# Performance work log

Hardware: AMD Instinct MI355X
Metric: run time of the kernel (lower is better)

The kernel has to match this reference:

```python
import jax, jax.numpy as jnp
import numpy as np
import math

H = 16
D_MODEL = 1024
D_K = D_MODEL // H
B, S = 4, 2048
NEG = -1.0e9


def setup_inputs() -> dict:
    key = jax.random.key(0)
    ks = jax.random.split(key, 13)
    scale = 1.0 / math.sqrt(D_MODEL)
    inp = {
        "query": jax.random.normal(ks[0], (B, S, D_MODEL), jnp.float32),
        "key": jax.random.normal(ks[1], (B, S, D_MODEL), jnp.float32),
        "value": jax.random.normal(ks[2], (B, S, D_MODEL), jnp.float32),
        "mask": jax.random.randint(ks[3], (B, S), 0, 2, jnp.int32),
        "Wq": jax.random.normal(ks[4], (D_MODEL, D_MODEL), jnp.float32) * scale,
        "bq": jax.random.normal(ks[5], (D_MODEL,), jnp.float32) * scale,
        "Wk": jax.random.normal(ks[6], (D_MODEL, D_MODEL), jnp.float32) * scale,
        "bk": jax.random.normal(ks[7], (D_MODEL,), jnp.float32) * scale,
        "Wv": jax.random.normal(ks[8], (D_MODEL, D_MODEL), jnp.float32) * scale,
        "bv": jax.random.normal(ks[9], (D_MODEL,), jnp.float32) * scale,
        "Wo": jax.random.normal(ks[10], (D_MODEL, D_MODEL), jnp.float32) * scale,
        "bo": jax.random.normal(ks[11], (D_MODEL,), jnp.float32) * scale,
    }
    return inp


def _split_heads(x):
    # [B, S, D] -> [B, H, S, D_K]
    b, s, _ = x.shape
    return x.reshape(b, s, H, D_K).transpose(0, 2, 1, 3)


def reference(query, key, value, mask, Wq, bq, Wk, bk, Wv, bv, Wo, bo):
    # torch nn.Linear: y = x @ W.T + b
    q = _split_heads(query @ Wq.T + bq)
    k = _split_heads(key @ Wk.T + bk)
    v = _split_heads(value @ Wv.T + bv)
    scores = jnp.einsum("bhqd,bhkd->bhqk", q, k) / math.sqrt(D_K)
    # [B, S] key-padding mask -> broadcast as [B, 1, 1, S] (== torch's [B,1,S,S] repeat)
    m = mask[:, None, None, :]
    scores = jnp.where(m == 0, NEG, scores)
    p = jax.nn.softmax(scores, axis=-1)
    out = jnp.einsum("bhqk,bhkd->bhqd", p, v)  # [B, H, S, D_K]
    out = out.transpose(0, 2, 1, 3).reshape(query.shape[0], -1, D_MODEL)
    return out @ Wo.T + bo
```

## Files before the change

### kernel.cpp

```cpp
#include <hip/hip_runtime.h>


#define DMODEL 1024
#define SLEN 2048
#define NHEAD 16
#define LOG2E 1.44269504088896340736f

typedef __attribute__((ext_vector_type(4))) float f32x4;
typedef __attribute__((ext_vector_type(8))) short bf16x8;
typedef __attribute__((ext_vector_type(4))) int i32x4;
typedef __attribute__((ext_vector_type(2))) int i32x2;

__device__ __forceinline__ unsigned short f2bf(float f) {
  __bf16 h = (__bf16)f;
  union { __bf16 h; unsigned short u; } cv; cv.h = h; return cv.u;
}
__device__ __forceinline__ unsigned pk(float a, float b) {
  return (unsigned)f2bf(a) | ((unsigned)f2bf(b) << 16);
}
__device__ __forceinline__ float fexp2(float x) {
#if __has_builtin(__builtin_amdgcn_exp2f)
  return __builtin_amdgcn_exp2f(x);
#else
  return exp2f(x);
#endif
}
__device__ __forceinline__ f32x4 zero4() {
  f32x4 z; z[0] = 0.f; z[1] = 0.f; z[2] = 0.f; z[3] = 0.f; return z;
}
__device__ __forceinline__ void gload16(const void* g, void* l) {
  __builtin_amdgcn_global_load_lds(
      (const __attribute__((address_space(1))) unsigned int*)(uintptr_t)g,
      (__attribute__((address_space(3))) unsigned int*)(uintptr_t)l, 16, 0, 0);
}

__global__ __launch_bounds__(256)
void gemm_qkv(const float* __restrict__ xq, const float* __restrict__ xk,
              const float* __restrict__ xv,
              const float* __restrict__ Wq, const float* __restrict__ bq,
              const float* __restrict__ Wk, const float* __restrict__ bk,
              const float* __restrict__ Wv, const float* __restrict__ bv,
              unsigned short* __restrict__ qw, unsigned short* __restrict__ kw,
              unsigned short* __restrict__ vw)
{
  const int z = blockIdx.z;
  const float* __restrict__ X    = (z == 0) ? xq : (z == 1) ? xk : xv;
  const float* __restrict__ W    = (z == 0) ? Wq : (z == 1) ? Wk : Wv;
  const float* __restrict__ bias = (z == 0) ? bq : (z == 1) ? bk : bv;
  const float scale = (z == 0) ? 0.125f * LOG2E : 1.0f;

  const int n0 = blockIdx.x * 128;
  const int m0 = blockIdx.y * 128;
  const int tid = threadIdx.x;
  const int lane = tid & 63, wid = tid >> 6;
  const int l15 = lane & 15, g = lane >> 4;
  const int wr = wid >> 1, wc = wid & 1;

  __shared__ __align__(16) unsigned short SM[2 * 128 * 40];
  unsigned short* Al = SM;
  unsigned short* Bl = SM + 128 * 40;
  unsigned short* TT = SM;

  const int srow = tid >> 1, sh = tid & 1;
  const float* __restrict__ Ag = X + (size_t)(m0 + srow) * DMODEL + sh * 16;
  const float* __restrict__ Bg = W + (size_t)(n0 + srow) * DMODEL + sh * 16;

  f32x4 acc[4][4];
#pragma unroll
  for (int i = 0; i < 4; ++i)
#pragma unroll
    for (int j = 0; j < 4; ++j) acc[i][j] = zero4();

  f32x4 ar[4], br[4];
#pragma unroll
  for (int i = 0; i < 4; ++i) {
    ar[i] = *(const f32x4*)(Ag + i * 4);
    br[i] = *(const f32x4*)(Bg + i * 4);
  }

  for (int kk = 0; kk < 32; ++kk) {
    __syncthreads();
    i32x4 wa0, wa1, wb0, wb1;
    wa0[0] = pk(ar[0][0], ar[0][1]); wa0[1] = pk(ar[0][2], ar[0][3]);
    wa0[2] = pk(ar[1][0], ar[1][1]); wa0[3] = pk(ar[1][2], ar[1][3]);
    wa1[0] = pk(ar[2][0], ar[2][1]); wa1[1] = pk(ar[2][2], ar[2][3]);
    wa1[2] = pk(ar[3][0], ar[3][1]); wa1[3] = pk(ar[3][2], ar[3][3]);
    wb0[0] = pk(br[0][0], br[0][1]); wb0[1] = pk(br[0][2], br[0][3]);
    wb0[2] = pk(br[1][0], br[1][1]); wb0[3] = pk(br[1][2], br[1][3]);
    wb1[0] = pk(br[2][0], br[2][1]); wb1[1] = pk(br[2][2], br[2][3]);
    wb1[2] = pk(br[3][0], br[3][1]); wb1[3] = pk(br[3][2], br[3][3]);
    *(i32x4*)&Al[srow * 40 + sh * 16]     = wa0;
    *(i32x4*)&Al[srow * 40 + sh * 16 + 8] = wa1;
    *(i32x4*)&Bl[srow * 40 + sh * 16]     = wb0;
    *(i32x4*)&Bl[srow * 40 + sh * 16 + 8] = wb1;
    __syncthreads();
    if (kk < 31) {
      const float* Ap = Ag + (kk + 1) * 32;
      const float* Bp = Bg + (kk + 1) * 32;
#pragma unroll
      for (int i = 0; i < 4; ++i) {
        ar[i] = *(const f32x4*)(Ap + i * 4);
        br[i] = *(const f32x4*)(Bp + i * 4);
      }
    }
    bf16x8 afr[4], bfr[4];
#pragma unroll
    for (int i = 0; i < 4; ++i) {
      afr[i] = *(const bf16x8*)&Al[(wr * 64 + i * 16 + l15) * 40 + g * 8];
      bfr[i] = *(const bf16x8*)&Bl[(wc * 64 + i * 16 + l15) * 40 + g * 8];
    }
#pragma unroll
    for (int mi = 0; mi < 4; ++mi)
#pragma unroll
      for (int ni = 0; ni < 4; ++ni)
        acc[mi][ni] = __builtin_amdgcn_mfma_f32_16x16x32_bf16(
            afr[mi], bfr[ni], acc[mi][ni], 0, 0, 0);
  }

  float bv4[4];
#pragma unroll
  for (int ni = 0; ni < 4; ++ni) bv4[ni] = bias[n0 + wc * 64 + ni * 16 + l15];

  if (z == 2) {
    const int bb = m0 >> 11, s0 = m0 & 2047;
#pragma unroll
    for (int p = 0; p < 2; ++p) {
      __syncthreads();
      if (wc == p) {
#pragma unroll
        for (int mi = 0; mi < 4; ++mi)
#pragma unroll
          for (int ni = 0; ni < 4; ++ni)
#pragma unroll
            for (int r = 0; r < 4; ++r)
              TT[(ni * 16 + l15) * 136 + wr * 64 + mi * 16 + 4 * g + r] =
                  f2bf(acc[mi][ni][r] + bv4[ni]);
      }
      __syncthreads();
      const int rr = tid >> 2, cc = (tid & 3) * 32;
      unsigned short* dp = vw + ((size_t)(bb * 1024 + n0 + p * 64 + rr)) * 2048 + s0 + cc;
      const unsigned short* sp = &TT[rr * 136 + cc];
#pragma unroll
      for (int j = 0; j < 4; ++j)
        *(i32x4*)(void*)(dp + j * 8) = *(const i32x4*)(const void*)(sp + j * 8);
    }
    return;
  }

  unsigned short* __restrict__ dst = (z == 0) ? qw : kw;
#pragma unroll
  for (int mi = 0; mi < 4; ++mi) {
#pragma unroll
    for (int ni = 0; ni < 4; ++ni) {
      const int n = n0 + wc * 64 + ni * 16 + l15;
      const int h = n >> 6, d = n & 63;
#pragma unroll
      for (int r = 0; r < 4; ++r) {
        const int m = m0 + wr * 64 + mi * 16 + 4 * g + r;
        const int b = m >> 11, s = m & 2047;
        const float val = (acc[mi][ni][r] + bv4[ni]) * scale;
        dst[((size_t)(b * NHEAD + h) * SLEN + s) * 64 + d] = f2bf(val);
      }
    }
  }
}

__global__ __launch_bounds__(256, 3)
void attn(const unsigned short* __restrict__ q_ws,
          const unsigned short* __restrict__ k_ws,
          const unsigned short* __restrict__ vT,
          const int* __restrict__ mask,
          unsigned short* __restrict__ o_ws)
{
  const int bh = blockIdx.x;
  const int qt = blockIdx.y;
  const int b = bh >> 4, h = bh & 15;
  const int tid = threadIdx.x, w = tid >> 6, lane = tid & 63;
  const int l15 = lane & 15, g = lane >> 4;

  __shared__ __align__(16) unsigned short Kb[2][64 * 64];
  __shared__ __align__(16) unsigned short Vb[2][64 * 64];
  __shared__ __align__(16) unsigned short Pl[4][16 * 64];
  __shared__ __align__(16) float maskf[2048];

  {
    const int4* mp = (const int4*)(mask + b * SLEN);
    const int4 ma = mp[tid * 2], mb = mp[tid * 2 + 1];
    float4 f0, f1;
    f0.x = ma.x ? 0.f : -1e9f; f0.y = ma.y ? 0.f : -1e9f;
    f0.z = ma.z ? 0.f : -1e9f; f0.w = ma.w ? 0.f : -1e9f;
    f1.x = mb.x ? 0.f : -1e9f; f1.y = mb.y ? 0.f : -1e9f;
    f1.z = mb.z ? 0.f : -1e9f; f1.w = mb.w ? 0.f : -1e9f;
    *(float4*)&maskf[tid * 8]     = f0;
    *(float4*)&maskf[tid * 8 + 4] = f1;
  }

  const size_t head = (size_t)bh * SLEN;
  const int r8 = lane >> 3, c8 = lane & 7;
  const int swz = ((c8 ^ r8) * 16);
  const unsigned pswz = (unsigned)((l15 & 7) << 4);

  const int qbase = qt * 128 + w * 32;
  bf16x8 qf[2][2];
  {
    const unsigned short* qp0 = q_ws + (head + qbase + l15) * 64;
    const unsigned short* qp1 = q_ws + (head + qbase + 16 + l15) * 64;
    qf[0][0] = *(const bf16x8*)(qp0 + g * 8);
    qf[0][1] = *(const bf16x8*)(qp0 + 32 + g * 8);
    qf[1][0] = *(const bf16x8*)(qp1 + g * 8);
    qf[1][1] = *(const bf16x8*)(qp1 + 32 + g * 8);
  }

  auto stage = [&](int kt2, int bufi) {
#pragma unroll
    for (int cl = 0; cl < 2; ++cl) {
      const int r = w * 16 + cl * 8 + r8;
      const char* gk = (const char*)(k_ws + (head + kt2 * 64 + r) * 64) + swz;
      gload16(gk, &Kb[bufi][(w * 16 + cl * 8) * 64]);
      const char* gv = (const char*)(vT + ((size_t)(bh * 64 + r)) * SLEN + kt2 * 64) + swz;
      gload16(gv, &Vb[bufi][(w * 16 + cl * 8) * 64]);
    }
  };

  stage(0, 0);
  __syncthreads();

  float m_run[2] = {-1e30f, -1e30f};
  float l_run[2] = {0.f, 0.f};
  f32x4 of[2][4];
#pragma unroll
  for (int qi = 0; qi < 2; ++qi)
#pragma unroll
    for (int n = 0; n < 4; ++n) of[qi][n] = zero4();

  unsigned short* Pw = (unsigned short*)Pl[w];
  int cur = 0;

  for (int kt = 0; kt < 32; ++kt) {
    if (kt + 1 < 32) stage(kt + 1, cur ^ 1);
    const char* Kc = (const char*)Kb[cur];
    const char* Vc = (const char*)Vb[cur];
    const int kv0 = kt * 64;

    f32x4 mv[4];
#pragma unroll
    for (int s = 0; s < 4; ++s) mv[s] = *(const f32x4*)&maskf[kv0 + s * 16 + g * 4];

#pragma unroll
    for (int qi = 0; qi < 2; ++qi) {
      f32x4 sac[4];
#pragma unroll
      for (int s = 0; s < 4; ++s) {
        const char* kr = Kc + (s * 16 + l15) * 128;
        const bf16x8 kf0 = *(const bf16x8*)(kr + ((unsigned)(g * 16) ^ pswz));
        const bf16x8 kf1 = *(const bf16x8*)(kr + ((unsigned)(64 + g * 16) ^ pswz));
        f32x4 zt = mv[s];
        zt = __builtin_amdgcn_mfma_f32_16x16x32_bf16(kf0, qf[qi][0], zt, 0, 0, 0);
        sac[s] = __builtin_amdgcn_mfma_f32_16x16x32_bf16(kf1, qf[qi][1], zt, 0, 0, 0);
      }

      float tmax = -3.0e38f;
#pragma unroll
      for (int s = 0; s < 4; ++s)
#pragma unroll
        for (int r = 0; r < 4; ++r) tmax = fmaxf(tmax, sac[s][r]);
      tmax = fmaxf(tmax, __shfl_xor(tmax, 16));
      tmax = fmaxf(tmax, __shfl_xor(tmax, 32));
      if (!__all(tmax <= m_run[qi] + 8.f)) {
        const float mnew = fmaxf(m_run[qi], tmax);
        const float alpha = fexp2(m_run[qi] - mnew);
        float af[4];
#pragma unroll
        for (int r = 0; r < 4; ++r) af[r] = __shfl(alpha, g * 4 + r);
#pragma unroll
        for (int n = 0; n < 4; ++n)
#pragma unroll
          for (int r = 0; r < 4; ++r) of[qi][n][r] *= af[r];
        l_run[qi] *= alpha;
        m_run[qi] = mnew;
      }
      float psum = 0.f;
      unsigned pr[4][2];
#pragma unroll
      for (int s = 0; s < 4; ++s) {
        const float p0 = fexp2(sac[s][0] - m_run[qi]);
        const float p1 = fexp2(sac[s][1] - m_run[qi]);
        const float p2 = fexp2(sac[s][2] - m_run[qi]);
        const float p3 = fexp2(sac[s][3] - m_run[qi]);
        psum += (p0 + p1) + (p2 + p3);
        pr[s][0] = pk(p0, p1); pr[s][1] = pk(p2, p3);
      }
      l_run[qi] += psum;
#pragma unroll
      for (int s = 0; s < 4; ++s) {
        i32x2 wv; wv[0] = (int)pr[s][0]; wv[1] = (int)pr[s][1];
        *(i32x2*)(void*)((char*)Pw + l15 * 128 + ((unsigned)(s * 32 + g * 8) ^ pswz)) = wv;
      }

#pragma unroll
      for (int k2 = 0; k2 < 2; ++k2) {
        const bf16x8 pa = *(const bf16x8*)(const void*)(
            (const char*)Pw + l15 * 128 + ((unsigned)(k2 * 64 + g * 16) ^ pswz));
#pragma unroll
        for (int n = 0; n < 4; ++n) {
          const bf16x8 vf = *(const bf16x8*)(
              Vc + (n * 16 + l15) * 128 + ((unsigned)(k2 * 64 + g * 16) ^ pswz));
          of[qi][n] = __builtin_amdgcn_mfma_f32_16x16x32_bf16(pa, vf, of[qi][n], 0, 0, 0);
        }
      }
    }
    __syncthreads();
    cur ^= 1;
  }

#pragma unroll
  for (int qi = 0; qi < 2; ++qi) {
    float lt = l_run[qi];
    lt += __shfl_xor(lt, 16);
    lt += __shfl_xor(lt, 32);
    float inv[4];
#pragma unroll
    for (int r = 0; r < 4; ++r) inv[r] = 1.f / __shfl(lt, g * 4 + r);
    const int qrow0 = qt * 128 + w * 32 + qi * 16;
#pragma unroll
    for (int n = 0; n < 4; ++n) {
      const int d = h * 64 + n * 16 + l15;
#pragma unroll
      for (int r = 0; r < 4; ++r) {
        const int sr = qrow0 + 4 * g + r;
        o_ws[((size_t)b * SLEN + sr) * DMODEL + d] = f2bf(of[qi][n][r] * inv[r]);
      }
    }
  }
}

__global__ __launch_bounds__(256)
void gemm_out(const unsigned short* __restrict__ ow,
              const float* __restrict__ Wo, const float* __restrict__ bo,
              float* __restrict__ out)
{
  const int n0 = blockIdx.x * 128;
  const int m0 = blockIdx.y * 128;
  const int tid = threadIdx.x;
  const int lane = tid & 63, wid = tid >> 6;
  const int l15 = lane & 15, g = lane >> 4;
  const int wr = wid >> 1, wc = wid & 1;

  __shared__ __align__(16) unsigned short Al[128 * 40];
  __shared__ __align__(16) unsigned short Bl[128 * 40];

  const int srow = tid >> 1, sh = tid & 1;
  const unsigned short* __restrict__ Ag = ow + (size_t)(m0 + srow) * DMODEL + sh * 16;
  const float* __restrict__ Bg = Wo + (size_t)(n0 + srow) * DMODEL + sh * 16;

  f32x4 acc[4][4];
#pragma unroll
  for (int i = 0; i < 4; ++i)
#pragma unroll
    for (int j = 0; j < 4; ++j) acc[i][j] = zero4();

  i32x4 ar0 = *(const i32x4*)Ag;
  i32x4 ar1 = *(const i32x4*)(Ag + 8);
  f32x4 br[4];
#pragma unroll
  for (int i = 0; i < 4; ++i) br[i] = *(const f32x4*)(Bg + i * 4);

  for (int kk = 0; kk < 32; ++kk) {
    __syncthreads();
    i32x4 wb0, wb1;
    wb0[0] = pk(br[0][0], br[0][1]); wb0[1] = pk(br[0][2], br[0][3]);
    wb0[2] = pk(br[1][0], br[1][1]); wb0[3] = pk(br[1][2], br[1][3]);
    wb1[0] = pk(br[2][0], br[2][1]); wb1[1] = pk(br[2][2], br[2][3]);
    wb1[2] = pk(br[3][0], br[3][1]); wb1[3] = pk(br[3][2], br[3][3]);
    *(i32x4*)&Al[srow * 40 + sh * 16]     = ar0;
    *(i32x4*)&Al[srow * 40 + sh * 16 + 8] = ar1;
    *(i32x4*)&Bl[srow * 40 + sh * 16]     = wb0;
    *(i32x4*)&Bl[srow * 40 + sh * 16 + 8] = wb1;
    __syncthreads();
    if (kk < 31) {
      const unsigned short* Ap = Ag + (kk + 1) * 32;
      const float* Bp = Bg + (kk + 1) * 32;
      ar0 = *(const i32x4*)Ap;
      ar1 = *(const i32x4*)(Ap + 8);
#pragma unroll
      for (int i = 0; i < 4; ++i) br[i] = *(const f32x4*)(Bp + i * 4);
    }
    bf16x8 afr[4], bfr[4];
#pragma unroll
    for (int i = 0; i < 4; ++i) {
      afr[i] = *(const bf16x8*)&Al[(wr * 64 + i * 16 + l15) * 40 + g * 8];
      bfr[i] = *(const bf16x8*)&Bl[(wc * 64 + i * 16 + l15) * 40 + g * 8];
    }
#pragma unroll
    for (int mi = 0; mi < 4; ++mi)
#pragma unroll
      for (int ni = 0; ni < 4; ++ni)
        acc[mi][ni] = __builtin_amdgcn_mfma_f32_16x16x32_bf16(
            afr[mi], bfr[ni], acc[mi][ni], 0, 0, 0);
  }

  float bv4[4];
#pragma unroll
  for (int ni = 0; ni < 4; ++ni) bv4[ni] = bo[n0 + wc * 64 + ni * 16 + l15];
#pragma unroll
  for (int mi = 0; mi < 4; ++mi) {
#pragma unroll
    for (int ni = 0; ni < 4; ++ni) {
      const int n = n0 + wc * 64 + ni * 16 + l15;
#pragma unroll
      for (int r = 0; r < 4; ++r) {
        const int m = m0 + wr * 64 + mi * 16 + 4 * g + r;
        out[(size_t)m * DMODEL + n] = acc[mi][ni][r] + bv4[ni];
      }
    }
  }
}

extern "C" void kernel_launch(void* const* d_in, const int* in_sizes, int n_in,
                              void* d_out, int out_size, void* d_ws, size_t ws_size,
                              hipStream_t stream) {
  const float* query = (const float*)d_in[0];
  const float* key_  = (const float*)d_in[1];
  const float* value = (const float*)d_in[2];
  const int*   mask  = (const int*)d_in[3];
  const float* Wq = (const float*)d_in[4];
  const float* bq = (const float*)d_in[5];
  const float* Wk = (const float*)d_in[6];
  const float* bk = (const float*)d_in[7];
  const float* Wv = (const float*)d_in[8];
  const float* bv = (const float*)d_in[9];
  const float* Wo = (const float*)d_in[10];
  const float* bo = (const float*)d_in[11];
  float* out = (float*)d_out;

  char* ws = (char*)d_ws;
  unsigned short* q_ws = (unsigned short*)(ws);
  unsigned short* k_ws = (unsigned short*)(ws + (size_t)16777216);
  unsigned short* vT   = (unsigned short*)(ws + (size_t)2 * 16777216);
  unsigned short* o_ws = (unsigned short*)(ws + (size_t)3 * 16777216);

  gemm_qkv<<<dim3(8, 64, 3), 256, 0, stream>>>(query, key_, value,
                                               Wq, bq, Wk, bk, Wv, bv,
                                               q_ws, k_ws, vT);
  attn<<<dim3(64, 16), 256, 0, stream>>>(q_ws, k_ws, vT, mask, o_ws);
  gemm_out<<<dim3(8, 64), 256, 0, stream>>>(o_ws, Wo, bo, out);
}
```

Before: 292.0 us.

## Deepen GEMM K-tile to 64 with XOR-swizzled LDS and XCD-aware block remap

Both projection GEMMs now stage a 64-wide K slice per iteration instead of 32, halving the number of barrier pairs. The padded LDS layout is replaced by an XOR swizzle on 16-byte chunks to avoid bank conflicts. A 1D grid with a remapped block index groups neighbouring tiles onto the same XCD for better L2 reuse. The cost is more registers for the prefetched data and double the LDS footprint, which may lower occupancy.

```diff
diff --git a/kernel.cpp b/kernel.cpp
--- a/kernel.cpp
+++ b/kernel.cpp
@@ -43,27 +43,33 @@
               unsigned short* __restrict__ qw, unsigned short* __restrict__ kw,
               unsigned short* __restrict__ vw)
 {
-  const int z = blockIdx.z;
+  const int bid = blockIdx.x;
+  const int wg = (bid & 7) * 192 + (bid >> 3);
+  const int z = wg >> 9;
+  const int r = wg & 511;
+  const int m0 = (r >> 3) * 128;
+  const int n0 = (r & 7) * 128;
+
   const float* __restrict__ X    = (z == 0) ? xq : (z == 1) ? xk : xv;
   const float* __restrict__ W    = (z == 0) ? Wq : (z == 1) ? Wk : Wv;
   const float* __restrict__ bias = (z == 0) ? bq : (z == 1) ? bk : bv;
   const float scale = (z == 0) ? 0.125f * LOG2E : 1.0f;
 
-  const int n0 = blockIdx.x * 128;
-  const int m0 = blockIdx.y * 128;
   const int tid = threadIdx.x;
   const int lane = tid & 63, wid = tid >> 6;
   const int l15 = lane & 15, g = lane >> 4;
   const int wr = wid >> 1, wc = wid & 1;
 
-  __shared__ __align__(16) unsigned short SM[2 * 128 * 40];
-  unsigned short* Al = SM;
-  unsigned short* Bl = SM + 128 * 40;
+  __shared__ __align__(16) unsigned short SM[2 * 128 * 64];
+  char* Al = (char*)SM;
+  char* Bl = (char*)(SM + 128 * 64);
   unsigned short* TT = SM;
 
-  const int srow = tid >> 1, sh = tid & 1;
-  const float* __restrict__ Ag = X + (size_t)(m0 + srow) * DMODEL + sh * 16;
-  const float* __restrict__ Bg = W + (size_t)(n0 + srow) * DMODEL + sh * 16;
+  const int arow = tid >> 1, ahalf = tid & 1;
+  const float* __restrict__ Ag = X + (size_t)(m0 + arow) * DMODEL + ahalf * 32;
+  const float* __restrict__ Bg = W + (size_t)(n0 + arow) * DMODEL + ahalf * 32;
+  const unsigned wswz = ((unsigned)(arow & 7)) << 4;
+  const unsigned rswz = ((unsigned)(l15 & 7)) << 4;
 
   f32x4 acc[4][4];
 #pragma unroll
@@ -71,50 +77,56 @@
 #pragma unroll
     for (int j = 0; j < 4; ++j) acc[i][j] = zero4();
 
-  f32x4 ar[4], br[4];
-#pragma unroll
-  for (int i = 0; i < 4; ++i) {
-    ar[i] = *(const f32x4*)(Ag + i * 4);
-    br[i] = *(const f32x4*)(Bg + i * 4);
-  }
-
-  for (int kk = 0; kk < 32; ++kk) {
+  f32x4 ar8[8], br8[8];
+#pragma unroll
+  for (int j = 0; j < 8; ++j) {
+    ar8[j] = *(const f32x4*)(Ag + j * 4);
+    br8[j] = *(const f32x4*)(Bg + j * 4);
+  }
+
+  for (int kt = 0; kt < 16; ++kt) {
     __syncthreads();
-    i32x4 wa0, wa1, wb0, wb1;
-    wa0[0] = pk(ar[0][0], ar[0][1]); wa0[1] = pk(ar[0][2], ar[0][3]);
-    wa0[2] = pk(ar[1][0], ar[1][1]); wa0[3] = pk(ar[1][2], ar[1][3]);
-    wa1[0] = pk(ar[2][0], ar[2][1]); wa1[1] = pk(ar[2][2], ar[2][3]);
-    wa1[2] = pk(ar[3][0], ar[3][1]); wa1[3] = pk(ar[3][2], ar[3][3]);
-    wb0[0] = pk(br[0][0], br[0][1]); wb0[1] = pk(br[0][2], br[0][3]);
-    wb0[2] = pk(br[1][0], br[1][1]); wb0[3] = pk(br[1][2], br[1][3]);
-    wb1[0] = pk(br[2][0], br[2][1]); wb1[1] = pk(br[2][2], br[2][3]);
-    wb1[2] = pk(br[3][0], br[3][1]); wb1[3] = pk(br[3][2], br[3][3]);
-    *(i32x4*)&Al[srow * 40 + sh * 16]     = wa0;
-    *(i32x4*)&Al[srow * 40 + sh * 16 + 8] = wa1;
-    *(i32x4*)&Bl[srow * 40 + sh * 16]     = wb0;
-    *(i32x4*)&Bl[srow * 40 + sh * 16 + 8] = wb1;
+#pragma unroll
+    for (int j = 0; j < 4; ++j) {
+      i32x4 wa, wb;
+      wa[0] = (int)pk(ar8[2*j][0], ar8[2*j][1]);
+      wa[1] = (int)pk(ar8[2*j][2], ar8[2*j][3]);
+      wa[2] = (int)pk(ar8[2*j+1][0], ar8[2*j+1][1]);
+      wa[3] = (int)pk(ar8[2*j+1][2], ar8[2*j+1][3]);
+      wb[0] = (int)pk(br8[2*j][0], br8[2*j][1]);
+      wb[1] = (int)pk(br8[2*j][2], br8[2*j][3]);
+      wb[2] = (int)pk(br8[2*j+1][0], br8[2*j+1][1]);
+      wb[3] = (int)pk(br8[2*j+1][2], br8[2*j+1][3]);
+      const unsigned off = (unsigned)(arow * 128) + (((unsigned)(ahalf * 64 + j * 16)) ^ wswz);
+      *(i32x4*)(Al + off) = wa;
+      *(i32x4*)(Bl + off) = wb;
+    }
     __syncthreads();
-    if (kk < 31) {
-      const float* Ap = Ag + (kk + 1) * 32;
-      const float* Bp = Bg + (kk + 1) * 32;
+    if (kt < 15) {
+      const float* Ap = Ag + (kt + 1) * 64;
+      const float* Bp = Bg + (kt + 1) * 64;
+#pragma unroll
+      for (int j = 0; j < 8; ++j) {
+        ar8[j] = *(const f32x4*)(Ap + j * 4);
+        br8[j] = *(const f32x4*)(Bp + j * 4);
+      }
+    }
+#pragma unroll
+    for (int kh = 0; kh < 2; ++kh) {
+      bf16x8 afr[4], bfr[4];
+      const unsigned cb = ((unsigned)(kh * 64 + g * 16)) ^ rswz;
 #pragma unroll
       for (int i = 0; i < 4; ++i) {
-        ar[i] = *(const f32x4*)(Ap + i * 4);
-        br[i] = *(const f32x4*)(Bp + i * 4);
-      }
-    }
-    bf16x8 afr[4], bfr[4];
-#pragma unroll
-    for (int i = 0; i < 4; ++i) {
-      afr[i] = *(const bf16x8*)&Al[(wr * 64 + i * 16 + l15) * 40 + g * 8];
-      bfr[i] = *(const bf16x8*)&Bl[(wc * 64 + i * 16 + l15) * 40 + g * 8];
-    }
-#pragma unroll
-    for (int mi = 0; mi < 4; ++mi)
-#pragma unroll
-      for (int ni = 0; ni < 4; ++ni)
-        acc[mi][ni] = __builtin_amdgcn_mfma_f32_16x16x32_bf16(
-            afr[mi], bfr[ni], acc[mi][ni], 0, 0, 0);
+        afr[i] = *(const bf16x8*)(Al + (wr * 64 + i * 16 + l15) * 128 + cb);
+        bfr[i] = *(const bf16x8*)(Bl + (wc * 64 + i * 16 + l15) * 128 + cb);
+      }
+#pragma unroll
+      for (int mi = 0; mi < 4; ++mi)
+#pragma unroll
+        for (int ni = 0; ni < 4; ++ni)
+          acc[mi][ni] = __builtin_amdgcn_mfma_f32_16x16x32_bf16(
+              afr[mi], bfr[ni], acc[mi][ni], 0, 0, 0);
+    }
   }
 
   float bv4[4];
@@ -132,9 +144,9 @@
 #pragma unroll
           for (int ni = 0; ni < 4; ++ni)
 #pragma unroll
-            for (int r = 0; r < 4; ++r)
-              TT[(ni * 16 + l15) * 136 + wr * 64 + mi * 16 + 4 * g + r] =
-                  f2bf(acc[mi][ni][r] + bv4[ni]);
+            for (int rr2 = 0; rr2 < 4; ++rr2)
+              TT[(ni * 16 + l15) * 136 + wr * 64 + mi * 16 + 4 * g + rr2] =
+                  f2bf(acc[mi][ni][rr2] + bv4[ni]);
       }
       __syncthreads();
       const int rr = tid >> 2, cc = (tid & 3) * 32;
@@ -155,10 +167,10 @@
       const int n = n0 + wc * 64 + ni * 16 + l15;
       const int h = n >> 6, d = n & 63;
 #pragma unroll
-      for (int r = 0; r < 4; ++r) {
-        const int m = m0 + wr * 64 + mi * 16 + 4 * g + r;
+      for (int rr2 = 0; rr2 < 4; ++rr2) {
+        const int m = m0 + wr * 64 + mi * 16 + 4 * g + rr2;
         const int b = m >> 11, s = m & 2047;
-        const float val = (acc[mi][ni][r] + bv4[ni]) * scale;
+        const float val = (acc[mi][ni][rr2] + bv4[ni]) * scale;
         dst[((size_t)(b * NHEAD + h) * SLEN + s) * 64 + d] = f2bf(val);
       }
     }
@@ -263,7 +275,7 @@
 #pragma unroll
       for (int s = 0; s < 4; ++s)
 #pragma unroll
-        for (int r = 0; r < 4; ++r) tmax = fmaxf(tmax, sac[s][r]);
+        for (int rr = 0; rr < 4; ++rr) tmax = fmaxf(tmax, sac[s][rr]);
       tmax = fmaxf(tmax, __shfl_xor(tmax, 16));
       tmax = fmaxf(tmax, __shfl_xor(tmax, 32));
       if (!__all(tmax <= m_run[qi] + 8.f)) {
@@ -271,11 +283,11 @@
         const float alpha = fexp2(m_run[qi] - mnew);
         float af[4];
 #pragma unroll
-        for (int r = 0; r < 4; ++r) af[r] = __shfl(alpha, g * 4 + r);
+        for (int rr = 0; rr < 4; ++rr) af[rr] = __shfl(alpha, g * 4 + rr);
 #pragma unroll
         for (int n = 0; n < 4; ++n)
 #pragma unroll
-          for (int r = 0; r < 4; ++r) of[qi][n][r] *= af[r];
+          for (int rr = 0; rr < 4; ++rr) of[qi][n][rr] *= af[rr];
         l_run[qi] *= alpha;
         m_run[qi] = mnew;
       }
@@ -320,15 +332,15 @@
     lt += __shfl_xor(lt, 32);
     float inv[4];
 #pragma unroll
-    for (int r = 0; r < 4; ++r) inv[r] = 1.f / __shfl(lt, g * 4 + r);
+    for (int rr = 0; rr < 4; ++rr) inv[rr] = 1.f / __shfl(lt, g * 4 + rr);
     const int qrow0 = qt * 128 + w * 32 + qi * 16;
 #pragma unroll
     for (int n = 0; n < 4; ++n) {
       const int d = h * 64 + n * 16 + l15;
 #pragma unroll
-      for (int r = 0; r < 4; ++r) {
-        const int sr = qrow0 + 4 * g + r;
-        o_ws[((size_t)b * SLEN + sr) * DMODEL + d] = f2bf(of[qi][n][r] * inv[r]);
+      for (int rr = 0; rr < 4; ++rr) {
+        const int sr = qrow0 + 4 * g + rr;
+        o_ws[((size_t)b * SLEN + sr) * DMODEL + d] = f2bf(of[qi][n][rr] * inv[rr]);
       }
     }
   }
@@ -339,19 +351,25 @@
               const float* __restrict__ Wo, const float* __restrict__ bo,
               float* __restrict__ out)
 {
-  const int n0 = blockIdx.x * 128;
-  const int m0 = blockIdx.y * 128;
+  const int bid = blockIdx.x;
+  const int wg = (bid & 7) * 64 + (bid >> 3);
+  const int m0 = (wg >> 3) * 128;
+  const int n0 = (wg & 7) * 128;
+
   const int tid = threadIdx.x;
   const int lane = tid & 63, wid = tid >> 6;
   const int l15 = lane & 15, g = lane >> 4;
   const int wr = wid >> 1, wc = wid & 1;
 
-  __shared__ __align__(16) unsigned short Al[128 * 40];
-  __shared__ __align__(16) unsigned short Bl[128 * 40];
-
-  const int srow = tid >> 1, sh = tid & 1;
-  const unsigned short* __restrict__ Ag = ow + (size_t)(m0 + srow) * DMODEL + sh * 16;
-  const float* __restrict__ Bg = Wo + (size_t)(n0 + srow) * DMODEL + sh * 16;
+  __shared__ __align__(16) unsigned short SM[2 * 128 * 64];
+  char* Al = (char*)SM;
+  char* Bl = (char*)(SM + 128 * 64);
+
+  const int arow = tid >> 1, ahalf = tid & 1;
+  const unsigned short* __restrict__ Ag = ow + (size_t)(m0 + arow) * DMODEL + ahalf * 32;
+  const float* __restrict__ Bg = Wo + (size_t)(n0 + arow) * DMODEL + ahalf * 32;
+  const unsigned wswz = ((unsigned)(arow & 7)) << 4;
+  const unsigned rswz = ((unsigned)(l15 & 7)) << 4;
 
   f32x4 acc[4][4];
 #pragma unroll
@@ -359,44 +377,51 @@
 #pragma unroll
     for (int j = 0; j < 4; ++j) acc[i][j] = zero4();
 
-  i32x4 ar0 = *(const i32x4*)Ag;
-  i32x4 ar1 = *(const i32x4*)(Ag + 8);
-  f32x4 br[4];
-#pragma unroll
-  for (int i = 0; i < 4; ++i) br[i] = *(const f32x4*)(Bg + i * 4);
-
-  for (int kk = 0; kk < 32; ++kk) {
+  i32x4 ar4[4];
+  f32x4 br8[8];
+#pragma unroll
+  for (int j = 0; j < 4; ++j) ar4[j] = *(const i32x4*)(Ag + j * 8);
+#pragma unroll
+  for (int j = 0; j < 8; ++j) br8[j] = *(const f32x4*)(Bg + j * 4);
+
+  for (int kt = 0; kt < 16; ++kt) {
     __syncthreads();
-    i32x4 wb0, wb1;
-    wb0[0] = pk(br[0][0], br[0][1]); wb0[1] = pk(br[0][2], br[0][3]);
-    wb0[2] = pk(br[1][0], br[1][1]); wb0[3] = pk(br[1][2], br[1][3]);
-    wb1[0] = pk(br[2][0], br[2][1]); wb1[1] = pk(br[2][2], br[2][3]);
-    wb1[2] = pk(br[3][0], br[3][1]); wb1[3] = pk(br[3][2], br[3][3]);
-    *(i32x4*)&Al[srow * 40 + sh * 16]     = ar0;
-    *(i32x4*)&Al[srow * 40 + sh * 16 + 8] = ar1;
-    *(i32x4*)&Bl[srow * 40 + sh * 16]     = wb0;
-    *(i32x4*)&Bl[srow * 40 + sh * 16 + 8] = wb1;
+#pragma unroll
+    for (int j = 0; j < 4; ++j) {
+      i32x4 wb;
+      wb[0] = (int)pk(br8[2*j][0], br8[2*j][1]);
+      wb[1] = (int)pk(br8[2*j][2], br8[2*j][3]);
+      wb[2] = (int)pk(br8[2*j+1][0], br8[2*j+1][1]);
+      wb[3] = (int)pk(br8[2*j+1][2], br8[2*j+1][3]);
+      const unsigned off = (unsigned)(arow * 128) + (((unsigned)(ahalf * 64 + j * 16)) ^ wswz);
+      *(i32x4*)(Al + off) = ar4[j];
+      *(i32x4*)(Bl + off) = wb;
+    }
     __syncthreads();
-    if (kk < 31) {
-      const unsigned short* Ap = Ag + (kk + 1) * 32;
-      const float* Bp = Bg + (kk + 1) * 32;
-      ar0 = *(const i32x4*)Ap;
-      ar1 = *(const i32x4*)(Ap + 8);
-#pragma unroll
-      for (int i = 0; i < 4; ++i) br[i] = *(const f32x4*)(Bp + i * 4);
-    }
-    bf16x8 afr[4], bfr[4];
-#pragma unroll
-    for (int i = 0; i < 4; ++i) {
-      afr[i] = *(const bf16x8*)&Al[(wr * 64 + i * 16 + l15) * 40 + g * 8];
-      bfr[i] = *(const bf16x8*)&Bl[(wc * 64 + i * 16 + l15) * 40 + g * 8];
-    }
-#pragma unroll
-    for (int mi = 0; mi < 4; ++mi)
-#pragma unroll
-      for (int ni = 0; ni < 4; ++ni)
-        acc[mi][ni] = __builtin_amdgcn_mfma_f32_16x16x32_bf16(
-            afr[mi], bfr[ni], acc[mi][ni], 0, 0, 0);
+    if (kt < 15) {
+      const unsigned short* Ap = Ag + (kt + 1) * 64;
+      const float* Bp = Bg + (kt + 1) * 64;
+#pragma unroll
+      for (int j = 0; j < 4; ++j) ar4[j] = *(const i32x4*)(Ap + j * 8);
+#pragma unroll
+      for (int j = 0; j < 8; ++j) br8[j] = *(const f32x4*)(Bp + j * 4);
+    }
+#pragma unroll
+    for (int kh = 0; kh < 2; ++kh) {
+      bf16x8 afr[4], bfr[4];
+      const unsigned cb = ((unsigned)(kh * 64 + g * 16)) ^ rswz;
+#pragma unroll
+      for (int i = 0; i < 4; ++i) {
+        afr[i] = *(const bf16x8*)(Al + (wr * 64 + i * 16 + l15) * 128 + cb);
+        bfr[i] = *(const bf16x8*)(Bl + (wc * 64 + i * 16 + l15) * 128 + cb);
+      }
+#pragma unroll
+      for (int mi = 0; mi < 4; ++mi)
+#pragma unroll
+        for (int ni = 0; ni < 4; ++ni)
+          acc[mi][ni] = __builtin_amdgcn_mfma_f32_16x16x32_bf16(
+              afr[mi], bfr[ni], acc[mi][ni], 0, 0, 0);
+    }
   }
 
   float bv4[4];
@@ -408,9 +433,9 @@
     for (int ni = 0; ni < 4; ++ni) {
       const int n = n0 + wc * 64 + ni * 16 + l15;
 #pragma unroll
-      for (int r = 0; r < 4; ++r) {
-        const int m = m0 + wr * 64 + mi * 16 + 4 * g + r;
-        out[(size_t)m * DMODEL + n] = acc[mi][ni][r] + bv4[ni];
+      for (int rr = 0; rr < 4; ++rr) {
+        const int m = m0 + wr * 64 + mi * 16 + 4 * g + rr;
+        out[(size_t)m * DMODEL + n] = acc[mi][ni][rr] + bv4[ni];
       }
     }
   }
@@ -439,9 +464,9 @@
   unsigned short* vT   = (unsigned short*)(ws + (size_t)2 * 16777216);
   unsigned short* o_ws = (unsigned short*)(ws + (size_t)3 * 16777216);
 
-  gemm_qkv<<<dim3(8, 64, 3), 256, 0, stream>>>(query, key_, value,
-                                               Wq, bq, Wk, bk, Wv, bv,
-                                               q_ws, k_ws, vT);
+  gemm_qkv<<<dim3(1536), 256, 0, stream>>>(query, key_, value,
+                                           Wq, bq, Wk, bk, Wv, bv,
+                                           q_ws, k_ws, vT);
   attn<<<dim3(64, 16), 256, 0, stream>>>(q_ws, k_ws, vT, mask, o_ws);
-  gemm_out<<<dim3(8, 64), 256, 0, stream>>>(o_ws, Wo, bo, out);
-}
+  gemm_out<<<dim3(512), 256, 0, stream>>>(o_ws, Wo, bo, out);
+}
```

After: 389.3 us. +33.3%, slower.
